# Kernel tuning notes

Measured on AMD Instinct MI355X. Metric: run time of the kernel, lower is better.

The kernel has to match this reference:

```python
import jax, jax.numpy as jnp
import numpy as np

B, M, D = 2048, 8192, 2048
SIM_THRESH = 0.5   # hard similarity cutoff (sims > 0.5)
ALPHA = 0.5        # dynamic threshold = mean - ALPHA * std
EPS = 1e-8         # torch cosine_similarity eps
NEG = -1e9         # masked-out logit for softmax


def setup_inputs() -> dict:
    key = jax.random.key(0)
    k1, k2, k3, k4 = jax.random.split(key, 4)
    query = jax.random.normal(k1, (B, D), jnp.float32)
    # Correlate memory bank with queries so cosine sims exceed the 0.5 threshold
    # for ~M/B entries per query (matched pairs have sim ~ 1/sqrt(1+0.75^2) ~ 0.8).
    idx = jax.random.randint(k2, (M,), 0, B)
    noise = jax.random.normal(k3, (M, D), jnp.float32)
    query_set = query[idx] + 0.75 * noise
    target_set = jax.random.normal(k4, (M, D), jnp.float32)
    return {"query": query, "query_set": query_set, "target_set": target_set}


def reference(query, query_set, target_set):
    # --- cosine similarity: [B, M] ---
    qn = query / jnp.maximum(jnp.linalg.norm(query, axis=-1, keepdims=True), EPS)
    sn = query_set / jnp.maximum(jnp.linalg.norm(query_set, axis=-1, keepdims=True), EPS)
    sims = jnp.einsum("bd,md->bm", qn, sn)  # [B, M]

    # --- first hard mask ---
    mask = sims > SIM_THRESH                              # [B, M]
    cnt = mask.sum(axis=-1)                               # [B]
    safe_cnt = jnp.maximum(cnt, 1).astype(sims.dtype)
    mean = jnp.where(mask, sims, 0.0).sum(-1) / safe_cnt  # masked mean  [B]
    var = (jnp.where(mask, (sims - mean[:, None]) ** 2, 0.0).sum(-1) / safe_cnt)
    std = jnp.sqrt(var)                                   # population std (unbiased=False)

    # --- dynamic threshold re-mask ---
    dyn_thr = mean - ALPHA * std                          # [B]
    final_mask = mask & (sims > dyn_thr[:, None])         # [B, M]
    fcnt = final_mask.sum(axis=-1)                        # [B]

    # --- softmax-weighted gather over surviving entries ---
    logits = jnp.where(final_mask, sims, NEG)
    w = jax.nn.softmax(logits, axis=-1)
    w = jnp.where(final_mask, w, 0.0)
    weighted = jnp.einsum("bm,md->bd", w, target_set)     # [B, D]

    # --- fallback 1: final mask empty -> target at argmin |sim - mean| ---
    closest = jnp.argmin(jnp.abs(sims - mean[:, None]), axis=-1)  # [B]
    fallback = target_set[closest]                        # [B, D]
    out = jnp.where((fcnt > 0)[:, None], weighted, fallback)

    # --- fallback 2: first mask empty -> zeros ---
    out = jnp.where((cnt > 0)[:, None], out, 0.0)
    return out
```

## Files before the change

kernel.cpp:

```cpp
#include <hip/hip_runtime.h>
#include <hip/hip_bf16.h>

#define B_DIM 2048
#define M_DIM 8192
#define D_DIM 2048
#define EPSN 1e-8f
#define ALPHA_C 0.5f
#define SIM_T 0.5f
#define QSCALE 800.0f
#define SCREEN_INT 121600
#define D_SCREEN 1024
#define CAP 2048

typedef __attribute__((ext_vector_type(4))) int i32x4;
typedef __attribute__((ext_vector_type(16))) int i32x16;

__global__ __launch_bounds__(256) void prep_kernel(const float* __restrict__ q,
                                                   const float* __restrict__ s,
                                                   signed char* __restrict__ A8,
                                                   signed char* __restrict__ B8,
                                                   float* __restrict__ rq,
                                                   float* __restrict__ rs,
                                                   int* __restrict__ ccnt) {
    const int row = blockIdx.x;
    const int tid = threadIdx.x;
    const float* src;
    signed char* dst;
    float* rdst;
    if (row < B_DIM) {
        src = q + (size_t)row * D_DIM; dst = A8 + (size_t)row * D_DIM; rdst = rq + row;
        if (tid == 0) ccnt[row] = 0;
    } else {
        int r = row - B_DIM;
        src = s + (size_t)r * D_DIM; dst = B8 + (size_t)r * D_DIM; rdst = rs + r;
    }
    const float4* src4 = (const float4*)src;
    float4 v0 = src4[2 * tid];
    float4 v1 = src4[2 * tid + 1];
    float acc = v0.x * v0.x + v0.y * v0.y + v0.z * v0.z + v0.w * v0.w
              + v1.x * v1.x + v1.y * v1.y + v1.z * v1.z + v1.w * v1.w;
    #pragma unroll
    for (int o = 32; o > 0; o >>= 1) acc += __shfl_down(acc, o, 64);
    __shared__ float red[4];
    if ((tid & 63) == 0) red[tid >> 6] = acc;
    __syncthreads();
    const float tot = red[0] + red[1] + red[2] + red[3];
    const float scale = 1.0f / fmaxf(sqrtf(tot), EPSN);
    if (tid == 0) *rdst = scale;

    const float qs = scale * QSCALE;
    float xs[8] = {v0.x * qs, v0.y * qs, v0.z * qs, v0.w * qs,
                   v1.x * qs, v1.y * qs, v1.z * qs, v1.w * qs};
    union { signed char b[8]; uint2 u; } pk;
    #pragma unroll
    for (int e = 0; e < 8; e++) {
        float c = fminf(fmaxf(xs[e], -127.f), 127.f);
        pk.b[e] = (signed char)(int)rintf(c);
    }
    ((uint2*)dst)[tid] = pk.u;
}

#define BKC 64
#define NCHUNK (D_SCREEN / BKC)
#define SLOT_SZ 32768

#define GLOAD_LDS16(g, l) \
    __builtin_amdgcn_global_load_lds((const __attribute__((address_space(1))) void*)(g), \
                                     (__attribute__((address_space(3))) void*)(l), 16, 0, 0)

#define STAGE(jj, l) GLOAD_LDS16(gsrc[l] + (size_t)(jj) * BKC, \
                                 lds + (((jj) & 3) * SLOT_SZ) + ldsDst[l])

__global__ __launch_bounds__(512, 2) void gemm_screen(const signed char* __restrict__ A8,
                                                      const signed char* __restrict__ B8,
                                                      int* __restrict__ ccnt,
                                                      int* __restrict__ cidx) {
    extern __shared__ unsigned char lds[];

    const int tid = threadIdx.x;
    const int wave = tid >> 6;
    const int lane = tid & 63;
    const int row0 = blockIdx.y * 256;
    const int col0 = blockIdx.x * 256;
    const int wm = (wave >> 2) * 128;
    const int wn = (wave & 3) * 64;

    i32x16 acc[4][2];
    #pragma unroll
    for (int i = 0; i < 4; i++)
        #pragma unroll
        for (int j = 0; j < 2; j++)
            #pragma unroll
            for (int r = 0; r < 16; r++) acc[i][j][r] = 0;

    const int Lr = lane >> 2;
    const int scn = (lane & 3) ^ ((lane >> 3) & 3);
    const signed char* gsrc[4];
    int ldsDst[4];
    #pragma unroll
    for (int l = 0; l < 4; l++) {
        const int r = (l & 1) * 128 + wave * 16 + Lr;
        const signed char* base = (l >> 1) ? (B8 + (size_t)(col0 + r) * D_DIM)
                                           : (A8 + (size_t)(row0 + r) * D_DIM);
        gsrc[l] = base + scn * 16;
        ldsDst[l] = (l >> 1) * 16384 + ((l & 1) * 128 + wave * 16) * 64;
    }

    const int r31 = lane & 31;
    const int hi = lane >> 5;
    const int swz = (r31 >> 1) & 3;

    #pragma unroll
    for (int j = 0; j < 3; j++) {
        STAGE(j, 0); STAGE(j, 1); STAGE(j, 2); STAGE(j, 3);
    }

    for (int j = 0; j < NCHUNK; j++) {
        if (j < NCHUNK - 2)       asm volatile("s_waitcnt vmcnt(8)" ::: "memory");
        else if (j == NCHUNK - 2) asm volatile("s_waitcnt vmcnt(4)" ::: "memory");
        else                      asm volatile("s_waitcnt vmcnt(0)" ::: "memory");
        __builtin_amdgcn_s_barrier();

        const unsigned char* sb = lds + (j & 3) * SLOT_SZ;
        const int js = j + 3;

        #pragma unroll
        for (int t = 0; t < 2; t++) {
            const int off = (((2 * t + hi) ^ swz) * 16);
            i32x4 afr[4], bfr[2];
            #pragma unroll
            for (int nj = 0; nj < 2; nj++)
                bfr[nj] = *(const i32x4*)(sb + 16384 + (wn + nj * 32 + r31) * 64 + off);
            #pragma unroll
            for (int i = 0; i < 4; i++)
                afr[i] = *(const i32x4*)(sb + (wm + i * 32 + r31) * 64 + off);
            if (js < NCHUNK) {
                if (t == 0) { STAGE(js, 0); STAGE(js, 1); }
                else        { STAGE(js, 2); STAGE(js, 3); }
            }
            __builtin_amdgcn_s_setprio(1);
            #pragma unroll
            for (int i = 0; i < 4; i++)
                #pragma unroll
                for (int nj = 0; nj < 2; nj++)
                    acc[i][nj] = __builtin_amdgcn_mfma_i32_32x32x32_i8(
                        afr[i], bfr[nj], acc[i][nj], 0, 0, 0);
            __builtin_amdgcn_s_setprio(0);
        }
    }

    #pragma unroll
    for (int nj = 0; nj < 2; nj++) {
        const int col = col0 + wn + nj * 32 + r31;
        #pragma unroll
        for (int i = 0; i < 4; i++) {
            const int rbase = row0 + wm + i * 32 + 4 * hi;
            #pragma unroll
            for (int r = 0; r < 16; r++) {
                if (acc[i][nj][r] > SCREEN_INT) {
                    const int row = rbase + (r & 3) + 8 * (r >> 2);
                    int pos = atomicAdd(&ccnt[row], 1);
                    if (pos < CAP) cidx[(size_t)row * CAP + pos] = col;
                }
            }
        }
    }
}

__device__ inline float wred_sum(float v) {
    #pragma unroll
    for (int o = 32; o > 0; o >>= 1) v += __shfl_down(v, o, 64);
    return v;
}
__device__ inline float wred_max(float v) {
    #pragma unroll
    for (int o = 32; o > 0; o >>= 1) v = fmaxf(v, __shfl_down(v, o, 64));
    return v;
}
__device__ inline int wred_sumi(int v) {
    #pragma unroll
    for (int o = 32; o > 0; o >>= 1) v += __shfl_down(v, o, 64);
    return v;
}
__device__ inline unsigned long long wred_minu64(unsigned long long v) {
    #pragma unroll
    for (int o = 32; o > 0; o >>= 1) {
        unsigned long long w = __shfl_down(v, o, 64);
        v = (w < v) ? w : v;
    }
    return v;
}

__global__ __launch_bounds__(256) void stats_gather(const float* __restrict__ q,
                                                    const float* __restrict__ s,
                                                    const float* __restrict__ T,
                                                    const float* __restrict__ rq,
                                                    const float* __restrict__ rs,
                                                    const int* __restrict__ ccnt,
                                                    const int* __restrict__ cidx,
                                                    float* __restrict__ out) {
    const int b = blockIdx.x;
    const int tid = threadIdx.x;
    const int lane = tid & 63, wave = tid >> 6;
    __shared__ float qrow[D_DIM];
    __shared__ float cval[CAP];
    __shared__ float rf[4], rg[4];
    __shared__ int ri[4];
    __shared__ unsigned long long ru[4];

    const int nc = min(ccnt[b], CAP);
    const float qscale = rq[b];

    {
        const float4* q4 = (const float4*)(q + (size_t)b * D_DIM);
        float4 v0 = q4[tid], v1 = q4[tid + 256];
        v0.x *= qscale; v0.y *= qscale; v0.z *= qscale; v0.w *= qscale;
        v1.x *= qscale; v1.y *= qscale; v1.z *= qscale; v1.w *= qscale;
        ((float4*)qrow)[tid] = v0;
        ((float4*)qrow)[tid + 256] = v1;
    }
    __syncthreads();

    const int* myidx = cidx + (size_t)b * CAP;
    for (int k = wave; k < nc; k += 4) {
        const int m = myidx[k];
        const float4* s4 = (const float4*)(s + (size_t)m * D_DIM);
        const float4* q4 = (const float4*)qrow;
        float p = 0.f;
        #pragma unroll
        for (int e = 0; e < 8; e++) {
            float4 sv = s4[lane + e * 64];
            float4 qv = q4[lane + e * 64];
            p = fmaf(sv.x, qv.x, p); p = fmaf(sv.y, qv.y, p);
            p = fmaf(sv.z, qv.z, p); p = fmaf(sv.w, qv.w, p);
        }
        p = wred_sum(p);
        if (lane == 0) cval[k] = p * rs[m];
    }
    __syncthreads();

    float psum = 0.f, pmax = -1e30f;
    int pcnt = 0;
    for (int k = tid; k < nc; k += 256) {
        float v = cval[k];
        if (v > SIM_T) { pcnt++; psum += v; pmax = fmaxf(pmax, v); }
    }
    psum = wred_sum(psum); pmax = wred_max(pmax); pcnt = wred_sumi(pcnt);
    if (lane == 0) { rf[wave] = psum; rg[wave] = pmax; ri[wave] = pcnt; }
    __syncthreads();
    const int cnt = ri[0] + ri[1] + ri[2] + ri[3];
    const float mean = (rf[0] + rf[1] + rf[2] + rf[3]) / (float)max(cnt, 1);
    const float mx = fmaxf(fmaxf(rg[0], rg[1]), fmaxf(rg[2], rg[3]));
    __syncthreads();

    float pvar = 0.f;
    unsigned long long pkey = 0xffffffffffffffffull;
    for (int k = tid; k < nc; k += 256) {
        float v = cval[k];
        if (v > SIM_T) { float d = v - mean; pvar += d * d; }
        unsigned long long kk = ((unsigned long long)__float_as_uint(fabsf(v - mean)) << 32)
                              | (unsigned)myidx[k];
        pkey = (kk < pkey) ? kk : pkey;
    }
    pvar = wred_sum(pvar); pkey = wred_minu64(pkey);
    if (lane == 0) { rf[wave] = pvar; ru[wave] = pkey; }
    __syncthreads();
    const float var = (rf[0] + rf[1] + rf[2] + rf[3]) / (float)max(cnt, 1);
    const float dyn = mean - ALPHA_C * sqrtf(var);
    unsigned long long k0 = ru[0] < ru[1] ? ru[0] : ru[1];
    unsigned long long k1 = ru[2] < ru[3] ? ru[2] : ru[3];
    const int closest = (int)(unsigned)((k0 < k1 ? k0 : k1) & 0xffffffffull);
    __syncthreads();

    float pden = 0.f;
    int pf = 0;
    for (int k = tid; k < nc; k += 256) {
        float v = cval[k];
        if (v > SIM_T && v > dyn) { pden += expf(v - mx); pf++; }
    }
    pden = wred_sum(pden); pf = wred_sumi(pf);
    if (lane == 0) { rf[wave] = pden; ri[wave] = pf; }
    __syncthreads();
    const float denom = rf[0] + rf[1] + rf[2] + rf[3];
    const int fcnt = ri[0] + ri[1] + ri[2] + ri[3];

    const float4* T4 = (const float4*)T;
    float4 a0 = make_float4(0.f, 0.f, 0.f, 0.f);
    float4 a1 = make_float4(0.f, 0.f, 0.f, 0.f);
    if (cnt == 0) {
    } else if (fcnt == 0) {
        a0 = T4[(size_t)closest * (D_DIM / 4) + tid];
        a1 = T4[(size_t)closest * (D_DIM / 4) + tid + 256];
    } else {
        const float rden = 1.0f / denom;
        for (int k = 0; k < nc; k++) {
            float v = cval[k];
            if (v > SIM_T && v > dyn) {
                const int m = myidx[k];
                const float w = expf(v - mx) * rden;
                float4 t0 = T4[(size_t)m * (D_DIM / 4) + tid];
                float4 t1 = T4[(size_t)m * (D_DIM / 4) + tid + 256];
                a0.x += w * t0.x; a0.y += w * t0.y; a0.z += w * t0.z; a0.w += w * t0.w;
                a1.x += w * t1.x; a1.y += w * t1.y; a1.z += w * t1.z; a1.w += w * t1.w;
            }
        }
    }
    float4* out4 = (float4*)(out + (size_t)b * D_DIM);
    out4[tid] = a0;
    out4[tid + 256] = a1;
}

extern "C" void kernel_launch(void* const* d_in, const int* in_sizes, int n_in,
                              void* d_out, int out_size, void* d_ws, size_t ws_size,
                              hipStream_t stream) {
    const float* query = (const float*)d_in[0];
    const float* qset  = (const float*)d_in[1];
    const float* tset  = (const float*)d_in[2];
    float* out = (float*)d_out;

    char* ws = (char*)d_ws;
    size_t off = 0;
    signed char* A8 = (signed char*)(ws + off); off += (size_t)B_DIM * D_DIM;
    signed char* B8 = (signed char*)(ws + off); off += (size_t)M_DIM * D_DIM;
    float* rq   = (float*)(ws + off);  off += B_DIM * sizeof(float);
    float* rs   = (float*)(ws + off);  off += M_DIM * sizeof(float);
    int* ccnt   = (int*)(ws + off);    off += B_DIM * sizeof(int);
    int* cidx   = (int*)(ws + off);    off += (size_t)B_DIM * CAP * sizeof(int);

    hipLaunchKernelGGL(prep_kernel, dim3(B_DIM + M_DIM), dim3(256), 0, stream,
                       query, qset, A8, B8, rq, rs, ccnt);
    hipLaunchKernelGGL(gemm_screen, dim3(M_DIM / 256, B_DIM / 256), dim3(512), 131072, stream,
                       A8, B8, ccnt, cidx);
    hipLaunchKernelGGL(stats_gather, dim3(B_DIM), dim3(256), 0, stream,
                       query, qset, tset, rq, rs, ccnt, cidx, out);
}
```

Before: 205.1 us.

## Map one query row per wavefront in stats_gather instead of per block

Restructures the stats/gather kernel so each 64-lane wavefront handles a whole query row, with four rows per block. Reductions use wave shuffles and no longer need shared-memory staging or __syncthreads. The query row is held in registers rather than shared memory. Each wave now serially recomputes all candidate dot products and gathers the target rows, so per-row latency rises and load can become imbalanced across waves with different candidate counts.

```diff
diff --git a/kernel.cpp b/kernel.cpp
--- a/kernel.cpp
+++ b/kernel.cpp
@@ -199,115 +199,100 @@
                                                     const int* __restrict__ ccnt,
                                                     const int* __restrict__ cidx,
                                                     float* __restrict__ out) {
-    const int b = blockIdx.x;
     const int tid = threadIdx.x;
     const int lane = tid & 63, wave = tid >> 6;
-    __shared__ float qrow[D_DIM];
-    __shared__ float cval[CAP];
-    __shared__ float rf[4], rg[4];
-    __shared__ int ri[4];
-    __shared__ unsigned long long ru[4];
+    const int b = blockIdx.x * 4 + wave;
+    __shared__ float cval[4][CAP];
 
     const int nc = min(ccnt[b], CAP);
     const float qscale = rq[b];
 
-    {
-        const float4* q4 = (const float4*)(q + (size_t)b * D_DIM);
-        float4 v0 = q4[tid], v1 = q4[tid + 256];
-        v0.x *= qscale; v0.y *= qscale; v0.z *= qscale; v0.w *= qscale;
-        v1.x *= qscale; v1.y *= qscale; v1.z *= qscale; v1.w *= qscale;
-        ((float4*)qrow)[tid] = v0;
-        ((float4*)qrow)[tid + 256] = v1;
-    }
-    __syncthreads();
+    const float4* q4 = (const float4*)(q + (size_t)b * D_DIM);
+    float4 qv[8];
+    #pragma unroll
+    for (int e = 0; e < 8; e++) {
+        float4 v = q4[lane + e * 64];
+        v.x *= qscale; v.y *= qscale; v.z *= qscale; v.w *= qscale;
+        qv[e] = v;
+    }
 
     const int* myidx = cidx + (size_t)b * CAP;
-    for (int k = wave; k < nc; k += 4) {
+    for (int k = 0; k < nc; k++) {
         const int m = myidx[k];
         const float4* s4 = (const float4*)(s + (size_t)m * D_DIM);
-        const float4* q4 = (const float4*)qrow;
         float p = 0.f;
         #pragma unroll
         for (int e = 0; e < 8; e++) {
             float4 sv = s4[lane + e * 64];
-            float4 qv = q4[lane + e * 64];
-            p = fmaf(sv.x, qv.x, p); p = fmaf(sv.y, qv.y, p);
-            p = fmaf(sv.z, qv.z, p); p = fmaf(sv.w, qv.w, p);
+            p = fmaf(sv.x, qv[e].x, p); p = fmaf(sv.y, qv[e].y, p);
+            p = fmaf(sv.z, qv[e].z, p); p = fmaf(sv.w, qv[e].w, p);
         }
         p = wred_sum(p);
-        if (lane == 0) cval[k] = p * rs[m];
-    }
-    __syncthreads();
+        if (lane == 0) cval[wave][k] = p * rs[m];
+    }
 
     float psum = 0.f, pmax = -1e30f;
     int pcnt = 0;
-    for (int k = tid; k < nc; k += 256) {
-        float v = cval[k];
+    for (int k = lane; k < nc; k += 64) {
+        float v = cval[wave][k];
         if (v > SIM_T) { pcnt++; psum += v; pmax = fmaxf(pmax, v); }
     }
     psum = wred_sum(psum); pmax = wred_max(pmax); pcnt = wred_sumi(pcnt);
-    if (lane == 0) { rf[wave] = psum; rg[wave] = pmax; ri[wave] = pcnt; }
-    __syncthreads();
-    const int cnt = ri[0] + ri[1] + ri[2] + ri[3];
-    const float mean = (rf[0] + rf[1] + rf[2] + rf[3]) / (float)max(cnt, 1);
-    const float mx = fmaxf(fmaxf(rg[0], rg[1]), fmaxf(rg[2], rg[3]));
-    __syncthreads();
+    const int cnt = __shfl(pcnt, 0, 64);
+    const float mean = __shfl(psum, 0, 64) / (float)max(cnt, 1);
+    const float mx = __shfl(pmax, 0, 64);
 
     float pvar = 0.f;
     unsigned long long pkey = 0xffffffffffffffffull;
-    for (int k = tid; k < nc; k += 256) {
-        float v = cval[k];
+    for (int k = lane; k < nc; k += 64) {
+        float v = cval[wave][k];
         if (v > SIM_T) { float d = v - mean; pvar += d * d; }
         unsigned long long kk = ((unsigned long long)__float_as_uint(fabsf(v - mean)) << 32)
                               | (unsigned)myidx[k];
         pkey = (kk < pkey) ? kk : pkey;
     }
     pvar = wred_sum(pvar); pkey = wred_minu64(pkey);
-    if (lane == 0) { rf[wave] = pvar; ru[wave] = pkey; }
-    __syncthreads();
-    const float var = (rf[0] + rf[1] + rf[2] + rf[3]) / (float)max(cnt, 1);
+    const float var = __shfl(pvar, 0, 64) / (float)max(cnt, 1);
     const float dyn = mean - ALPHA_C * sqrtf(var);
-    unsigned long long k0 = ru[0] < ru[1] ? ru[0] : ru[1];
-    unsigned long long k1 = ru[2] < ru[3] ? ru[2] : ru[3];
-    const int closest = (int)(unsigned)((k0 < k1 ? k0 : k1) & 0xffffffffull);
-    __syncthreads();
+    const int closest = (int)(unsigned)(__shfl(pkey, 0, 64) & 0xffffffffull);
 
     float pden = 0.f;
     int pf = 0;
-    for (int k = tid; k < nc; k += 256) {
-        float v = cval[k];
+    for (int k = lane; k < nc; k += 64) {
+        float v = cval[wave][k];
         if (v > SIM_T && v > dyn) { pden += expf(v - mx); pf++; }
     }
     pden = wred_sum(pden); pf = wred_sumi(pf);
-    if (lane == 0) { rf[wave] = pden; ri[wave] = pf; }
-    __syncthreads();
-    const float denom = rf[0] + rf[1] + rf[2] + rf[3];
-    const int fcnt = ri[0] + ri[1] + ri[2] + ri[3];
+    const float denom = __shfl(pden, 0, 64);
+    const int fcnt = __shfl(pf, 0, 64);
 
     const float4* T4 = (const float4*)T;
-    float4 a0 = make_float4(0.f, 0.f, 0.f, 0.f);
-    float4 a1 = make_float4(0.f, 0.f, 0.f, 0.f);
+    float4 a[8];
+    #pragma unroll
+    for (int e = 0; e < 8; e++) a[e] = make_float4(0.f, 0.f, 0.f, 0.f);
     if (cnt == 0) {
     } else if (fcnt == 0) {
-        a0 = T4[(size_t)closest * (D_DIM / 4) + tid];
-        a1 = T4[(size_t)closest * (D_DIM / 4) + tid + 256];
+        #pragma unroll
+        for (int e = 0; e < 8; e++) a[e] = T4[(size_t)closest * (D_DIM / 4) + lane + e * 64];
     } else {
         const float rden = 1.0f / denom;
         for (int k = 0; k < nc; k++) {
-            float v = cval[k];
+            float v = cval[wave][k];
             if (v > SIM_T && v > dyn) {
                 const int m = myidx[k];
                 const float w = expf(v - mx) * rden;
-                float4 t0 = T4[(size_t)m * (D_DIM / 4) + tid];
-                float4 t1 = T4[(size_t)m * (D_DIM / 4) + tid + 256];
-                a0.x += w * t0.x; a0.y += w * t0.y; a0.z += w * t0.z; a0.w += w * t0.w;
-                a1.x += w * t1.x; a1.y += w * t1.y; a1.z += w * t1.z; a1.w += w * t1.w;
+                #pragma unroll
+                for (int e = 0; e < 8; e++) {
+                    float4 t = T4[(size_t)m * (D_DIM / 4) + lane + e * 64];
+                    a[e].x += w * t.x; a[e].y += w * t.y;
+                    a[e].z += w * t.z; a[e].w += w * t.w;
+                }
             }
         }
     }
     float4* out4 = (float4*)(out + (size_t)b * D_DIM);
-    out4[tid] = a0;
-    out4[tid + 256] = a1;
+    #pragma unroll
+    for (int e = 0; e < 8; e++) out4[lane + e * 64] = a[e];
 }
 
 extern "C" void kernel_launch(void* const* d_in, const int* in_sizes, int n_in,
@@ -331,6 +316,6 @@
                        query, qset, A8, B8, rq, rs, ccnt);
     hipLaunchKernelGGL(gemm_screen, dim3(M_DIM / 256, B_DIM / 256), dim3(512), 131072, stream,
                        A8, B8, ccnt, cidx);
-    hipLaunchKernelGGL(stats_gather, dim3(B_DIM), dim3(256), 0, stream,
+    hipLaunchKernelGGL(stats_gather, dim3(B_DIM / 4), dim3(256), 0, stream,
                        query, qset, tset, rq, rs, ccnt, cidx, out);
 }
```

Result: no change. 208.8 us (+1.8%).
